# Performance work log

Hardware: AMD Instinct MI355X
Metric: run time of the kernel (lower is better)

The kernel has to match this reference:

```python
import jax, jax.numpy as jnp
import numpy as np

WIDTH = 64  # attention_width

def setup_inputs() -> dict:
    key = jax.random.key(0)
    ks = jax.random.split(key, 4)
    B, T, D, U = 4, 1024, 1024, 64
    x = jax.random.normal(ks[0], (B, T, D), dtype=jnp.float32)
    Wt = jax.random.normal(ks[1], (D, U), dtype=jnp.float32) * (1.0 / np.sqrt(D))
    Wx = jax.random.normal(ks[2], (D, U), dtype=jnp.float32) * (1.0 / np.sqrt(D))
    bh = jnp.zeros((U,), dtype=jnp.float32)
    Wa = jax.random.normal(ks[3], (U, 1), dtype=jnp.float32) * (1.0 / np.sqrt(U))
    ba = jnp.zeros((1,), dtype=jnp.float32)
    return {"x": x, "Wt": Wt, "Wx": Wx, "bh": bh, "Wa": Wa, "ba": ba}


def reference(x, Wt, Wx, bh, Wa, ba):
    B, T, D = x.shape
    # additive emission: h = tanh(q_i + k_j + bh), e_ij = h @ Wa + ba
    q = jnp.einsum('btd,du->btu', x, Wt)  # [B,T,U]
    k = jnp.einsum('btd,du->btu', x, Wx)  # [B,T,U]
    h = jnp.tanh(q[:, :, None, :] + k[:, None, :, :] + bh)  # [B,T,T,U]
    e = jnp.einsum('btsu,uo->bts', h, Wa) + ba[0]  # [B,T,T]
    # local-width band mask (width centered, history_only=False)
    idx = jnp.arange(T)
    lower = (idx - WIDTH // 2)[:, None]           # [T,1]
    upper = lower + WIDTH
    band = (lower <= idx[None, :]) & (idx[None, :] < upper)  # [T,T]
    e = e - 10000.0 * (1.0 - band.astype(e.dtype))
    a = jax.nn.softmax(e, axis=-1)  # [B,T,T]
    v = jnp.einsum('bts,bsd->btd', a, x)
    return v
```

## Files before the change

kernel.cpp:

```cpp
#include <hip/hip_runtime.h>

#define BB 4
#define TT 1024
#define DD 1024
#define UU 64
#define HW 32

__device__ __forceinline__ float tanh_fast(float x) {
  float ax = __builtin_fabsf(x);
  float t = __expf(-2.0f * ax);
  float r = (1.0f - t) * __builtin_amdgcn_rcpf(1.0f + t);
  return __builtin_copysignf(r, x);
}

__global__ __launch_bounds__(512) void proj_kernel(
    const float* __restrict__ x, const float* __restrict__ Wt,
    const float* __restrict__ Wx, float* __restrict__ qo, float* __restrict__ ko)
{
  __shared__ __align__(16) float xs[8 * DD];
  __shared__ __align__(16) float red[8][1024];

  const int tid  = threadIdx.x;
  const int row0 = blockIdx.x * 8;

  {
    const float4* src = (const float4*)(x + (size_t)row0 * DD);
    float4* dst = (float4*)xs;
    #pragma unroll
    for (int i = 0; i < 4; ++i) dst[tid + 512 * i] = src[tid + 512 * i];
  }
  __syncthreads();

  const int u2  = tid & 31;
  const int sel = (tid >> 5) & 1;
  const int kq  = tid >> 6;
  const float* __restrict__ W = sel ? Wx : Wt;
  const float* __restrict__ Wp = W + 2 * u2;

  float acc0[8], acc1[8];
  #pragma unroll
  for (int r = 0; r < 8; ++r) { acc0[r] = 0.f; acc1[r] = 0.f; }

  const int dbeg = kq * 128;
  #pragma unroll 4
  for (int dc = dbeg; dc < dbeg + 128; dc += 4) {
    float2 w0 = *(const float2*)(Wp + (size_t)(dc + 0) * UU);
    float2 w1 = *(const float2*)(Wp + (size_t)(dc + 1) * UU);
    float2 w2 = *(const float2*)(Wp + (size_t)(dc + 2) * UU);
    float2 w3 = *(const float2*)(Wp + (size_t)(dc + 3) * UU);
    #pragma unroll
    for (int r = 0; r < 8; ++r) {
      float4 xv = *(const float4*)(xs + r * DD + dc);
      acc0[r] += xv.x * w0.x + xv.y * w1.x + xv.z * w2.x + xv.w * w3.x;
      acc1[r] += xv.x * w0.y + xv.y * w1.y + xv.z * w2.y + xv.w * w3.y;
    }
  }

  {
    #pragma unroll
    for (int r = 0; r < 8; ++r) {
      *(float2*)(&red[kq][(sel * 8 + r) * 64 + 2 * u2]) = make_float2(acc0[r], acc1[r]);
    }
  }
  __syncthreads();

  #pragma unroll
  for (int m = 0; m < 2; ++m) {
    int oi = tid + 512 * m;
    float v = 0.f;
    #pragma unroll
    for (int p = 0; p < 8; ++p) v += red[p][oi];
    int c  = oi & 63;
    int r  = (oi >> 6) & 7;
    int so = oi >> 9;
    float* dst = so ? ko : qo;
    dst[(size_t)(row0 + r) * UU + c] = v;
  }
}

__global__ __launch_bounds__(512) void band_kernel(
    const float* __restrict__ x,  const float* __restrict__ qi,
    const float* __restrict__ ki, const float* __restrict__ bh,
    const float* __restrict__ Wa, const float* __restrict__ ba,
    float* __restrict__ out)
{
  __shared__ __align__(16) float qpb[8 * UU];
  __shared__ __align__(16) float ks[72 * UU];
  __shared__ __align__(16) float at[72 * 8];

  const int tid  = threadIdx.x;
  const int bid  = blockIdx.x;
  const int tile = (bid & 7) * 64 + (bid >> 3);
  const int b    = tile >> 7;
  const int i0   = (tile & 127) * 8;

  const int jlo = max(0, i0 - HW);
  const int jhi = min(TT, i0 + 8 - 1 + HW);
  const int NJ  = jhi - jlo;

  {
    if (tid < 128) {
      float4 qv = ((const float4*)(qi + (size_t)(b * TT + i0) * UU))[tid];
      float4 bv = ((const float4*)bh)[tid & 15];
      qv.x += bv.x; qv.y += bv.y; qv.z += bv.z; qv.w += bv.w;
      ((float4*)qpb)[tid] = qv;
    }
    const float4* ksrc = (const float4*)(ki + (size_t)(b * TT + jlo) * UU);
    float4* kdst = (float4*)ks;
    const int nk4 = NJ * (UU / 4);
    for (int i2 = tid; i2 < nk4; i2 += 512) kdst[i2] = ksrc[i2];
  }
  __syncthreads();

  const float bav = ba[0];

  {
    const int w    = tid >> 6;
    const int lane = tid & 63;
    const int g    = lane >> 3;
    const int uc   = (lane & 7) * 8;
    float qv[8], wv[8];
    #pragma unroll
    for (int s = 0; s < 8; ++s) qv[s] = qpb[g * UU + uc + s];
    {
      float4 wa0 = *(const float4*)(Wa + uc);
      float4 wa1 = *(const float4*)(Wa + uc + 4);
      wv[0] = wa0.x; wv[1] = wa0.y; wv[2] = wa0.z; wv[3] = wa0.w;
      wv[4] = wa1.x; wv[5] = wa1.y; wv[6] = wa1.z; wv[7] = wa1.w;
    }
    const int ig = i0 + g;
    for (int j = w; j < NJ; j += 8) {
      const float* kp = ks + j * UU + uc;
      float s0 = 0.f;
      #pragma unroll
      for (int s = 0; s < 8; ++s) {
        float z = qv[s] + kp[s];
        s0 += tanh_fast(z) * wv[s];
      }
      s0 += __shfl_xor(s0, 1);
      s0 += __shfl_xor(s0, 2);
      s0 += __shfl_xor(s0, 4);
      const int jg = jlo + j;
      const bool inband = (jg >= ig - HW) && (jg < ig + HW);
      if ((lane & 7) == 0) at[j * 8 + g] = inband ? (s0 + bav) : -1e30f;
    }
  }
  __syncthreads();

  {
    const int row = tid >> 6;
    const int l   = tid & 63;
    float v0 = (l      < NJ) ? at[(l     ) * 8 + row] : -1e30f;
    float v1 = (l + 64 < NJ) ? at[(l + 64) * 8 + row] : -1e30f;
    float m = fmaxf(v0, v1);
    #pragma unroll
    for (int off = 32; off >= 1; off >>= 1) m = fmaxf(m, __shfl_xor(m, off));
    float e0 = __expf(v0 - m);
    float e1 = __expf(v1 - m);
    float ssum = e0 + e1;
    #pragma unroll
    for (int off = 32; off >= 1; off >>= 1) ssum += __shfl_xor(ssum, off);
    float inv = 1.0f / ssum;
    if (l      < NJ) at[(l     ) * 8 + row] = e0 * inv;
    if (l + 64 < NJ) at[(l + 64) * 8 + row] = e1 * inv;
  }
  __syncthreads();

  {
    float2 vacc[8];
    #pragma unroll
    for (int i = 0; i < 8; ++i) vacc[i] = make_float2(0.f, 0.f);
    const float* xb = x + (size_t)(b * TT + jlo) * DD + 2 * tid;
    #pragma unroll 2
    for (int j = 0; j < NJ; ++j) {
      float2 xv = *(const float2*)(xb + (size_t)j * DD);
      float4 a0 = *(const float4*)(at + j * 8);
      float4 a1 = *(const float4*)(at + j * 8 + 4);
      float av[8] = {a0.x, a0.y, a0.z, a0.w, a1.x, a1.y, a1.z, a1.w};
      #pragma unroll
      for (int i = 0; i < 8; ++i) {
        vacc[i].x = __builtin_fmaf(av[i], xv.x, vacc[i].x);
        vacc[i].y = __builtin_fmaf(av[i], xv.y, vacc[i].y);
      }
    }
    float* ob = out + (size_t)(b * TT + i0) * DD + 2 * tid;
    #pragma unroll
    for (int i = 0; i < 8; ++i) *(float2*)(ob + (size_t)i * DD) = vacc[i];
  }
}

extern "C" void kernel_launch(void* const* d_in, const int* in_sizes, int n_in,
                              void* d_out, int out_size, void* d_ws, size_t ws_size,
                              hipStream_t stream) {
  const float* x  = (const float*)d_in[0];
  const float* Wt = (const float*)d_in[1];
  const float* Wx = (const float*)d_in[2];
  const float* bh = (const float*)d_in[3];
  const float* Wa = (const float*)d_in[4];
  const float* ba = (const float*)d_in[5];
  float* out = (float*)d_out;

  float* q = (float*)d_ws;
  float* k = q + (size_t)BB * TT * UU;

  proj_kernel<<<dim3((BB * TT) / 8), dim3(512), 0, stream>>>(x, Wt, Wx, q, k);
  band_kernel<<<dim3((BB * TT) / 8), dim3(512), 0, stream>>>(x, q, k, bh, Wa, ba, out);
}
```

Baseline: 122.3 us.

## Process 16 rows per projection block and software-prefetch weights and x rows

The projection kernel now handles 16 rows per block instead of 8, reusing each weight load across twice as many rows and halving the grid. Shared memory is merged into one 64KB buffer, reused for the cross-warp reduction. Weight loads and the band kernel's x/attention loads are software-prefetched one iteration ahead to hide latency. The larger tile raises register and LDS use, which may cut occupancy, and there are only 256 blocks left to spread across the CUs.

```diff
diff --git a/kernel.cpp b/kernel.cpp
--- a/kernel.cpp
+++ b/kernel.cpp
@@ -17,64 +17,72 @@
     const float* __restrict__ x, const float* __restrict__ Wt,
     const float* __restrict__ Wx, float* __restrict__ qo, float* __restrict__ ko)
 {
-  __shared__ __align__(16) float xs[8 * DD];
-  __shared__ __align__(16) float red[8][1024];
+  __shared__ __align__(16) float smem[16 * DD];
 
   const int tid  = threadIdx.x;
-  const int row0 = blockIdx.x * 8;
+  const int row0 = blockIdx.x * 16;
 
   {
     const float4* src = (const float4*)(x + (size_t)row0 * DD);
-    float4* dst = (float4*)xs;
-    #pragma unroll
-    for (int i = 0; i < 4; ++i) dst[tid + 512 * i] = src[tid + 512 * i];
+    float4* dst = (float4*)smem;
+    #pragma unroll
+    for (int i = 0; i < 8; ++i) dst[tid + 512 * i] = src[tid + 512 * i];
   }
   __syncthreads();
 
   const int u2  = tid & 31;
   const int sel = (tid >> 5) & 1;
-  const int kq  = tid >> 6;
-  const float* __restrict__ W = sel ? Wx : Wt;
-  const float* __restrict__ Wp = W + 2 * u2;
-
-  float acc0[8], acc1[8];
+  const int w8  = tid >> 6;
+  const float* __restrict__ Wp = (sel ? Wx : Wt) + 2 * u2;
+
+  float acc0[16], acc1[16];
   #pragma unroll
-  for (int r = 0; r < 8; ++r) { acc0[r] = 0.f; acc1[r] = 0.f; }
-
-  const int dbeg = kq * 128;
-  #pragma unroll 4
-  for (int dc = dbeg; dc < dbeg + 128; dc += 4) {
-    float2 w0 = *(const float2*)(Wp + (size_t)(dc + 0) * UU);
-    float2 w1 = *(const float2*)(Wp + (size_t)(dc + 1) * UU);
-    float2 w2 = *(const float2*)(Wp + (size_t)(dc + 2) * UU);
-    float2 w3 = *(const float2*)(Wp + (size_t)(dc + 3) * UU);
-    #pragma unroll
-    for (int r = 0; r < 8; ++r) {
-      float4 xv = *(const float4*)(xs + r * DD + dc);
-      acc0[r] += xv.x * w0.x + xv.y * w1.x + xv.z * w2.x + xv.w * w3.x;
-      acc1[r] += xv.x * w0.y + xv.y * w1.y + xv.z * w2.y + xv.w * w3.y;
-    }
-  }
-
-  {
-    #pragma unroll
-    for (int r = 0; r < 8; ++r) {
-      *(float2*)(&red[kq][(sel * 8 + r) * 64 + 2 * u2]) = make_float2(acc0[r], acc1[r]);
+  for (int r = 0; r < 16; ++r) { acc0[r] = 0.f; acc1[r] = 0.f; }
+
+  const int dbeg = w8 * 128;
+  const int dend = dbeg + 128;
+
+  float2 wn0 = *(const float2*)(Wp + (size_t)(dbeg + 0) * UU);
+  float2 wn1 = *(const float2*)(Wp + (size_t)(dbeg + 1) * UU);
+  float2 wn2 = *(const float2*)(Wp + (size_t)(dbeg + 2) * UU);
+  float2 wn3 = *(const float2*)(Wp + (size_t)(dbeg + 3) * UU);
+
+  for (int dc = dbeg; dc < dend; dc += 4) {
+    float2 w0 = wn0, w1 = wn1, w2 = wn2, w3 = wn3;
+    if (dc + 4 < dend) {
+      wn0 = *(const float2*)(Wp + (size_t)(dc + 4) * UU);
+      wn1 = *(const float2*)(Wp + (size_t)(dc + 5) * UU);
+      wn2 = *(const float2*)(Wp + (size_t)(dc + 6) * UU);
+      wn3 = *(const float2*)(Wp + (size_t)(dc + 7) * UU);
+    }
+    #pragma unroll
+    for (int r = 0; r < 16; ++r) {
+      float4 xv = *(const float4*)(smem + r * DD + dc);
+      acc0[r] = __builtin_fmaf(xv.x, w0.x, __builtin_fmaf(xv.y, w1.x,
+                __builtin_fmaf(xv.z, w2.x, __builtin_fmaf(xv.w, w3.x, acc0[r]))));
+      acc1[r] = __builtin_fmaf(xv.x, w0.y, __builtin_fmaf(xv.y, w1.y,
+                __builtin_fmaf(xv.z, w2.y, __builtin_fmaf(xv.w, w3.y, acc1[r]))));
     }
   }
   __syncthreads();
 
   #pragma unroll
-  for (int m = 0; m < 2; ++m) {
+  for (int r = 0; r < 16; ++r) {
+    *(float2*)(smem + w8 * 2048 + r * 128 + sel * 64 + 2 * u2) =
+        make_float2(acc0[r], acc1[r]);
+  }
+  __syncthreads();
+
+  #pragma unroll
+  for (int m = 0; m < 4; ++m) {
     int oi = tid + 512 * m;
     float v = 0.f;
     #pragma unroll
-    for (int p = 0; p < 8; ++p) v += red[p][oi];
-    int c  = oi & 63;
-    int r  = (oi >> 6) & 7;
-    int so = oi >> 9;
-    float* dst = so ? ko : qo;
-    dst[(size_t)(row0 + r) * UU + c] = v;
+    for (int p = 0; p < 8; ++p) v += smem[p * 2048 + oi];
+    int r = oi >> 7;
+    int c = oi & 127;
+    float* dst = (c < 64) ? qo : ko;
+    dst[(size_t)(row0 + r) * UU + (c & 63)] = v;
   }
 }
 
@@ -171,11 +179,19 @@
     #pragma unroll
     for (int i = 0; i < 8; ++i) vacc[i] = make_float2(0.f, 0.f);
     const float* xb = x + (size_t)(b * TT + jlo) * DD + 2 * tid;
-    #pragma unroll 2
+
+    float2 xn = *(const float2*)(xb);
+    float4 an0 = *(const float4*)(at);
+    float4 an1 = *(const float4*)(at + 4);
+
     for (int j = 0; j < NJ; ++j) {
-      float2 xv = *(const float2*)(xb + (size_t)j * DD);
-      float4 a0 = *(const float4*)(at + j * 8);
-      float4 a1 = *(const float4*)(at + j * 8 + 4);
+      float2 xv = xn;
+      float4 a0 = an0, a1 = an1;
+      if (j + 1 < NJ) {
+        xn  = *(const float2*)(xb + (size_t)(j + 1) * DD);
+        an0 = *(const float4*)(at + (j + 1) * 8);
+        an1 = *(const float4*)(at + (j + 1) * 8 + 4);
+      }
       float av[8] = {a0.x, a0.y, a0.z, a0.w, a1.x, a1.y, a1.z, a1.w};
       #pragma unroll
       for (int i = 0; i < 8; ++i) {
@@ -203,6 +219,6 @@
   float* q = (float*)d_ws;
   float* k = q + (size_t)BB * TT * UU;
 
-  proj_kernel<<<dim3((BB * TT) / 8), dim3(512), 0, stream>>>(x, Wt, Wx, q, k);
+  proj_kernel<<<dim3((BB * TT) / 16), dim3(512), 0, stream>>>(x, Wt, Wx, q, k);
   band_kernel<<<dim3((BB * TT) / 8), dim3(512), 0, stream>>>(x, q, k, bh, Wa, ba, out);
 }
```

Result: slower. 127.6 us (+4.4%).

## Fuse projection and band kernels via cooperative launch with grid sync

Applied to the files above, without the earlier changes.

Merges the projection and band-attention kernels into one cooperative kernel, separated by a grid-wide barrier, and keeps the original two-kernel launch as a fallback if the cooperative launch fails. The proj phase now uses explicit FMA chains, and the band weighted-sum loop software-prefetches the next x row and attention weights. The aim is to remove the second launch and the gap between kernels, and to let x stay warm in cache between phases. In exchange, all 512 blocks of 64KB shared memory must be co-resident, the grid barrier adds its own cost, and the band phase now runs with the larger shared-memory footprint.

```diff
diff --git a/kernel.cpp b/kernel.cpp
--- a/kernel.cpp
+++ b/kernel.cpp
@@ -1,4 +1,7 @@
 #include <hip/hip_runtime.h>
+#include <hip/hip_cooperative_groups.h>
+
+namespace cg = cooperative_groups;
 
 #define BB 4
 #define TT 1024
@@ -13,15 +16,15 @@
   return __builtin_copysignf(r, x);
 }
 
-__global__ __launch_bounds__(512) void proj_kernel(
+__device__ __forceinline__ void proj_phase(
+    float* __restrict__ smem, int tile,
     const float* __restrict__ x, const float* __restrict__ Wt,
     const float* __restrict__ Wx, float* __restrict__ qo, float* __restrict__ ko)
 {
-  __shared__ __align__(16) float xs[8 * DD];
-  __shared__ __align__(16) float red[8][1024];
-
   const int tid  = threadIdx.x;
-  const int row0 = blockIdx.x * 8;
+  const int row0 = tile * 8;
+  float* xs  = smem;
+  float* red = smem + 8192;
 
   {
     const float4* src = (const float4*)(x + (size_t)row0 * DD);
@@ -34,8 +37,7 @@
   const int u2  = tid & 31;
   const int sel = (tid >> 5) & 1;
   const int kq  = tid >> 6;
-  const float* __restrict__ W = sel ? Wx : Wt;
-  const float* __restrict__ Wp = W + 2 * u2;
+  const float* __restrict__ Wp = (sel ? Wx : Wt) + 2 * u2;
 
   float acc0[8], acc1[8];
   #pragma unroll
@@ -51,16 +53,17 @@
     #pragma unroll
     for (int r = 0; r < 8; ++r) {
       float4 xv = *(const float4*)(xs + r * DD + dc);
-      acc0[r] += xv.x * w0.x + xv.y * w1.x + xv.z * w2.x + xv.w * w3.x;
-      acc1[r] += xv.x * w0.y + xv.y * w1.y + xv.z * w2.y + xv.w * w3.y;
-    }
-  }
-
-  {
-    #pragma unroll
-    for (int r = 0; r < 8; ++r) {
-      *(float2*)(&red[kq][(sel * 8 + r) * 64 + 2 * u2]) = make_float2(acc0[r], acc1[r]);
-    }
+      acc0[r] = __builtin_fmaf(xv.x, w0.x, __builtin_fmaf(xv.y, w1.x,
+                __builtin_fmaf(xv.z, w2.x, __builtin_fmaf(xv.w, w3.x, acc0[r]))));
+      acc1[r] = __builtin_fmaf(xv.x, w0.y, __builtin_fmaf(xv.y, w1.y,
+                __builtin_fmaf(xv.z, w2.y, __builtin_fmaf(xv.w, w3.y, acc1[r]))));
+    }
+  }
+
+  #pragma unroll
+  for (int r = 0; r < 8; ++r) {
+    *(float2*)(red + kq * 1024 + (sel * 8 + r) * 64 + 2 * u2) =
+        make_float2(acc0[r], acc1[r]);
   }
   __syncthreads();
 
@@ -69,7 +72,7 @@
     int oi = tid + 512 * m;
     float v = 0.f;
     #pragma unroll
-    for (int p = 0; p < 8; ++p) v += red[p][oi];
+    for (int p = 0; p < 8; ++p) v += red[p * 1024 + oi];
     int c  = oi & 63;
     int r  = (oi >> 6) & 7;
     int so = oi >> 9;
@@ -78,21 +81,20 @@
   }
 }
 
-__global__ __launch_bounds__(512) void band_kernel(
+__device__ __forceinline__ void band_phase(
+    float* __restrict__ smem, int tile,
     const float* __restrict__ x,  const float* __restrict__ qi,
     const float* __restrict__ ki, const float* __restrict__ bh,
     const float* __restrict__ Wa, const float* __restrict__ ba,
     float* __restrict__ out)
 {
-  __shared__ __align__(16) float qpb[8 * UU];
-  __shared__ __align__(16) float ks[72 * UU];
-  __shared__ __align__(16) float at[72 * 8];
-
-  const int tid  = threadIdx.x;
-  const int bid  = blockIdx.x;
-  const int tile = (bid & 7) * 64 + (bid >> 3);
-  const int b    = tile >> 7;
-  const int i0   = (tile & 127) * 8;
+  float* qpb = smem;
+  float* ks  = smem + 512;
+  float* at  = smem + 5120;
+
+  const int tid = threadIdx.x;
+  const int b   = tile >> 7;
+  const int i0  = (tile & 127) * 8;
 
   const int jlo = max(0, i0 - HW);
   const int jhi = min(TT, i0 + 8 - 1 + HW);
@@ -171,11 +173,19 @@
     #pragma unroll
     for (int i = 0; i < 8; ++i) vacc[i] = make_float2(0.f, 0.f);
     const float* xb = x + (size_t)(b * TT + jlo) * DD + 2 * tid;
-    #pragma unroll 2
+
+    float2 xn  = *(const float2*)(xb);
+    float4 an0 = *(const float4*)(at);
+    float4 an1 = *(const float4*)(at + 4);
+
     for (int j = 0; j < NJ; ++j) {
-      float2 xv = *(const float2*)(xb + (size_t)j * DD);
-      float4 a0 = *(const float4*)(at + j * 8);
-      float4 a1 = *(const float4*)(at + j * 8 + 4);
+      float2 xv = xn;
+      float4 a0 = an0, a1 = an1;
+      if (j + 1 < NJ) {
+        xn  = *(const float2*)(xb + (size_t)(j + 1) * DD);
+        an0 = *(const float4*)(at + (j + 1) * 8);
+        an1 = *(const float4*)(at + (j + 1) * 8 + 4);
+      }
       float av[8] = {a0.x, a0.y, a0.z, a0.w, a1.x, a1.y, a1.z, a1.w};
       #pragma unroll
       for (int i = 0; i < 8; ++i) {
@@ -187,6 +197,40 @@
     #pragma unroll
     for (int i = 0; i < 8; ++i) *(float2*)(ob + (size_t)i * DD) = vacc[i];
   }
+}
+
+__global__ __launch_bounds__(512, 4) void fused_kernel(
+    const float* __restrict__ x,  const float* __restrict__ Wt,
+    const float* __restrict__ Wx, const float* __restrict__ bh,
+    const float* __restrict__ Wa, const float* __restrict__ ba,
+    float* __restrict__ out, float* __restrict__ q, float* __restrict__ k)
+{
+  __shared__ __align__(16) float smem[16384];
+  const int bid  = blockIdx.x;
+  const int tile = (bid & 7) * 64 + (bid >> 3);
+  proj_phase(smem, tile, x, Wt, Wx, q, k);
+  cg::this_grid().sync();
+  band_phase(smem, tile, x, q, k, bh, Wa, ba, out);
+}
+
+__global__ __launch_bounds__(512) void proj_kernel(
+    const float* __restrict__ x, const float* __restrict__ Wt,
+    const float* __restrict__ Wx, float* __restrict__ q, float* __restrict__ k)
+{
+  __shared__ __align__(16) float smem[16384];
+  proj_phase(smem, blockIdx.x, x, Wt, Wx, q, k);
+}
+
+__global__ __launch_bounds__(512) void band_kernel(
+    const float* __restrict__ x,  const float* __restrict__ qi,
+    const float* __restrict__ ki, const float* __restrict__ bh,
+    const float* __restrict__ Wa, const float* __restrict__ ba,
+    float* __restrict__ out)
+{
+  __shared__ __align__(16) float smem[5696];
+  const int bid  = blockIdx.x;
+  const int tile = (bid & 7) * 64 + (bid >> 3);
+  band_phase(smem, tile, x, qi, ki, bh, Wa, ba, out);
 }
 
 extern "C" void kernel_launch(void* const* d_in, const int* in_sizes, int n_in,
@@ -203,6 +247,13 @@
   float* q = (float*)d_ws;
   float* k = q + (size_t)BB * TT * UU;
 
-  proj_kernel<<<dim3((BB * TT) / 8), dim3(512), 0, stream>>>(x, Wt, Wx, q, k);
-  band_kernel<<<dim3((BB * TT) / 8), dim3(512), 0, stream>>>(x, q, k, bh, Wa, ba, out);
-}
+  void* args[] = {(void*)&x, (void*)&Wt, (void*)&Wx, (void*)&bh, (void*)&Wa,
+                  (void*)&ba, (void*)&out, (void*)&q, (void*)&k};
+  hipError_t err = hipLaunchCooperativeKernel((const void*)fused_kernel,
+                                              dim3((BB * TT) / 8), dim3(512),
+                                              args, 0, stream);
+  if (err != hipSuccess) {
+    proj_kernel<<<dim3((BB * TT) / 8), dim3(512), 0, stream>>>(x, Wt, Wx, q, k);
+    band_kernel<<<dim3((BB * TT) / 8), dim3(512), 0, stream>>>(x, q, k, bh, Wa, ba, out);
+  }
+}
```

Result: slower. 194.9 us (+59.4%).
